# Performance work log

Measured on AMD Instinct MI355X. Metric: run time of the kernel, lower is better.

## Reference

```python
import jax, jax.numpy as jnp
import numpy as np

B, T, D, H = 32, 4096, 512, 512


def setup_inputs() -> dict:
    key = jax.random.key(0)
    ks = jax.random.split(key, 8)
    s = 1.0 / np.sqrt(D)
    return {
        "hidden_state": jax.random.normal(ks[0], (B, D), jnp.float32),
        "encoder_outputs": jax.random.normal(ks[1], (B, T, D), jnp.float32),
        "W": jax.random.normal(ks[2], (D, H), jnp.float32) * s,
        "U": jax.random.normal(ks[3], (D, H), jnp.float32) * s,
        "V": jax.random.normal(ks[4], (H,), jnp.float32) * s,
        "bias": jnp.zeros((H,), jnp.float32),
        "Wa": jax.random.normal(ks[5], (H, H), jnp.float32) * (1.0 / np.sqrt(H)),
        "ba": jnp.zeros((H,), jnp.float32),
    }


def reference(hidden_state, encoder_outputs, W, U, V, bias, Wa, ba):
    # dens1: [B,1,H] ; dens2: [B,T,H]
    dens1 = jnp.einsum('bd,dh->bh', hidden_state, W)[:, None, :]
    dens2 = jnp.einsum('btd,dh->bth', encoder_outputs, U)
    pre = dens1 + dens2 + bias                       # [B,T,H]
    tanh_ = jnp.tanh(jnp.einsum('bth,hk->btk', pre, Wa) + ba)  # extra Dense(tanh)
    cij = jnp.einsum('bth,h->bt', tanh_, V)          # [B,T]
    alphas = jax.nn.softmax(cij, axis=-1)            # [B,T]
    output = jnp.einsum('btd,bt->bd', encoder_outputs, alphas)  # weighted sum
    return output, alphas
```

## Files before the change

### kernel.cpp

```cpp
#include <hip/hip_runtime.h>
#include <hip/hip_bf16.h>


#define BB 32
#define TT 4096
#define DD 512
#define HH 512
#define BK 64

typedef short s16x8 __attribute__((ext_vector_type(8)));
typedef float f32x4 __attribute__((ext_vector_type(4)));

union FU { float f; unsigned u; };

static __device__ __forceinline__ unsigned pack_bf16_trunc(float a, float b) {
    FU ua, ub; ua.f = a; ub.f = b;
    return (ua.u >> 16) | (ub.u & 0xffff0000u);
}

static __device__ __forceinline__ unsigned short f2bf_rne(float x) {
    FU v; v.f = x;
    unsigned u = v.u;
    u = u + 0x7fffu + ((u >> 16) & 1u);
    return (unsigned short)(u >> 16);
}

static __device__ __forceinline__ float tanh_fast(float x) {
    float e = __expf(2.0f * x);
    return 1.0f - 2.0f * __builtin_amdgcn_rcpf(e + 1.0f);
}

static __device__ __forceinline__ void gload_lds16(const void* g, void* l) {
    __builtin_amdgcn_global_load_lds(
        (const __attribute__((address_space(1))) unsigned int*)g,
        (__attribute__((address_space(3))) unsigned int*)l, 16, 0, 0);
}

__global__ void k_dens1(const float* __restrict__ hs, const float* __restrict__ W,
                        const float* __restrict__ bias, float* __restrict__ g) {
    int bi = blockIdx.x;
    int dc = bi & 3, hb = (bi >> 2) & 1, b = bi >> 3;
    int h = hb * 256 + threadIdx.x;
    float s = (dc == 0) ? bias[h] : 0.0f;
    int d0 = dc * 128;
    #pragma unroll 4
    for (int d = 0; d < 128; ++d)
        s = fmaf(hs[b * DD + d0 + d], W[(size_t)(d0 + d) * HH + h], s);
    atomicAdd(&g[b * HH + h], s);
}

__global__ void k_cvec(const float* __restrict__ g, const float* __restrict__ Wa,
                       const float* __restrict__ ba, float* __restrict__ cvec) {
    int bi = blockIdx.x;
    int hc = bi & 3, kb = (bi >> 2) & 1, b = bi >> 3;
    int k = kb * 256 + threadIdx.x;
    float s = (hc == 0) ? ba[k] : 0.0f;
    int h0 = hc * 128;
    #pragma unroll 4
    for (int h = 0; h < 128; ++h)
        s = fmaf(g[b * HH + h0 + h], Wa[(size_t)(h0 + h) * HH + k], s);
    atomicAdd(&cvec[b * HH + k], s);
}

__global__ void k_uwa(const float* __restrict__ U, const float* __restrict__ Wa,
                      unsigned short* __restrict__ UWaT) {
    int d0 = blockIdx.x * 8;
    int tid = threadIdx.x;
    __shared__ float Us[8][DD];
    #pragma unroll
    for (int i = 0; i < 16; ++i) {
        int idx = i * 256 + tid;
        Us[idx >> 9][idx & 511] = U[(size_t)(d0 + (idx >> 9)) * HH + (idx & 511)];
    }
    __syncthreads();
    float acc[8][2] = {};
    #pragma unroll 2
    for (int h = 0; h < DD; ++h) {
        float w0 = Wa[(size_t)h * HH + tid];
        float w1 = Wa[(size_t)h * HH + 256 + tid];
        #pragma unroll
        for (int dd = 0; dd < 8; ++dd) {
            float u = Us[dd][h];
            acc[dd][0] = fmaf(u, w0, acc[dd][0]);
            acc[dd][1] = fmaf(u, w1, acc[dd][1]);
        }
    }
    #pragma unroll
    for (int dd = 0; dd < 8; ++dd) {
        UWaT[(size_t)tid * DD + d0 + dd] = f2bf_rne(acc[dd][0]);
        UWaT[(size_t)(tid + 256) * DD + d0 + dd] = f2bf_rne(acc[dd][1]);
    }
}

__global__ void __launch_bounds__(512, 2) k_gemm_tanh(
    const float* __restrict__ e, const unsigned short* __restrict__ Bt,
    const float* __restrict__ cvec, const float* __restrict__ V,
    float* __restrict__ cij) {
    int tid = threadIdx.x;
    int m0 = blockIdx.x * 128;
    int lane = tid & 63, w = tid >> 6;
    int wr = w >> 2, wc = w & 3;
    int wm = wr * 64, wn = wc * 128;
    int lcol = lane & 15, q = lane >> 4;
    int rl = lane >> 3, gg = lane & 7;

    __shared__ __align__(16) unsigned short As[128 * BK];
    __shared__ __align__(16) unsigned short Bs[512 * BK];

    f32x4 acc[4][8] = {};

    const float* Abase = e + (size_t)m0 * DD;

    for (int k0 = 0; k0 < DD; k0 += BK) {
        float4 av[4];
        #pragma unroll
        for (int it = 0; it < 4; ++it) {
            int idx = it * 512 + tid;
            int row = idx >> 4, c4 = idx & 15;
            av[it] = *(const float4*)(Abase + (size_t)row * DD + k0 + c4 * 4);
        }
        #pragma unroll
        for (int u = 0; u < 8; ++u) {
            int n0 = w * 64 + u * 8;
            const unsigned short* gp =
                Bt + (size_t)(n0 + rl) * DD + k0 + ((gg ^ rl) << 3);
            gload_lds16(gp, &Bs[n0 * 64]);
        }
        #pragma unroll
        for (int it = 0; it < 4; ++it) {
            int idx = it * 512 + tid;
            int row = idx >> 4, c4 = idx & 15;
            uint2 wv;
            wv.x = pack_bf16_trunc(av[it].x, av[it].y);
            wv.y = pack_bf16_trunc(av[it].z, av[it].w);
            int g = c4 >> 1, half = c4 & 1;
            *(uint2*)&As[(g * 128 + (row ^ g)) * 8 + half * 4] = wv;
        }
        __syncthreads();
        #pragma unroll
        for (int ks = 0; ks < BK; ks += 32) {
            int gk = ks >> 3;
            s16x8 af[4], bfr[8];
            #pragma unroll
            for (int i = 0; i < 4; ++i) {
                int row = wm + i * 16 + lcol, g = gk + q;
                af[i] = *(const s16x8*)&As[(g * 128 + (row ^ g)) * 8];
            }
            #pragma unroll
            for (int j = 0; j < 8; ++j) {
                int col = wn + j * 16 + lcol, g = gk + q;
                bfr[j] = *(const s16x8*)&Bs[col * 64 + ((g ^ (col & 7)) << 3)];
            }
            #pragma unroll
            for (int i = 0; i < 4; ++i)
                #pragma unroll
                for (int j = 0; j < 8; ++j)
                    acc[i][j] = __builtin_amdgcn_mfma_f32_16x16x32_bf16(
                        af[i], bfr[j], acc[i][j], 0, 0, 0);
        }
        __syncthreads();
    }

    int b = m0 >> 12;
    float cvv[8], Vv[8];
    #pragma unroll
    for (int j = 0; j < 8; ++j) {
        int h = wn + j * 16 + lcol;
        cvv[j] = cvec[b * HH + h];
        Vv[j] = V[h];
    }
    #pragma unroll
    for (int i = 0; i < 4; ++i) {
        #pragma unroll
        for (int r = 0; r < 4; ++r) {
            float s = 0.0f;
            #pragma unroll
            for (int j = 0; j < 8; ++j)
                s = fmaf(tanh_fast(acc[i][j][r] + cvv[j]), Vv[j], s);
            s += __shfl_xor(s, 1);
            s += __shfl_xor(s, 2);
            s += __shfl_xor(s, 4);
            s += __shfl_xor(s, 8);
            if (lcol == 0)
                atomicAdd(&cij[m0 + wm + i * 16 + q * 4 + r], s);
        }
    }
}

__global__ void k_softmax(const float* __restrict__ cij, float* __restrict__ alphas) {
    int b = blockIdx.x, tid = threadIdx.x;
    const float* row = cij + (size_t)b * TT;
    __shared__ float red[4];
    float m = -1e30f;
    for (int t = tid; t < TT; t += 256) m = fmaxf(m, row[t]);
    #pragma unroll
    for (int o = 1; o < 64; o <<= 1) m = fmaxf(m, __shfl_xor(m, o));
    if ((tid & 63) == 0) red[tid >> 6] = m;
    __syncthreads();
    m = fmaxf(fmaxf(red[0], red[1]), fmaxf(red[2], red[3]));
    __syncthreads();
    float sum = 0.0f;
    for (int t = tid; t < TT; t += 256) sum += __expf(row[t] - m);
    #pragma unroll
    for (int o = 1; o < 64; o <<= 1) sum += __shfl_xor(sum, o);
    if ((tid & 63) == 0) red[tid >> 6] = sum;
    __syncthreads();
    float inv = 1.0f / (red[0] + red[1] + red[2] + red[3]);
    for (int t = tid; t < TT; t += 256)
        alphas[(size_t)b * TT + t] = __expf(row[t] - m) * inv;
}

__global__ void k_wsum(const float* __restrict__ e, const float* __restrict__ alphas,
                       float* __restrict__ pw) {
    int b = blockIdx.x >> 6;
    int chunk = blockIdx.x & 63;
    int t0 = chunk * 64;
    int tid = threadIdx.x;
    int half = tid >> 7, f4 = tid & 127;
    const float* base = e + (size_t)b * TT * DD;
    const float* al = alphas + (size_t)b * TT;
    f32x4 a0 = {0, 0, 0, 0}, a1 = {0, 0, 0, 0};
    for (int it = 0; it < 16; ++it) {
        int t = t0 + it * 4 + half;
        float w0 = al[t], w1 = al[t + 2];
        f32x4 v0 = *(const f32x4*)(base + (size_t)t * DD + f4 * 4);
        f32x4 v1 = *(const f32x4*)(base + (size_t)(t + 2) * DD + f4 * 4);
        a0 += w0 * v0;
        a1 += w1 * v1;
    }
    a0 += a1;
    __shared__ f32x4 red[128];
    if (half == 1) red[f4] = a0;
    __syncthreads();
    if (half == 0) {
        a0 += red[f4];
        *(f32x4*)&pw[((size_t)(b * 64 + chunk)) * DD + f4 * 4] = a0;
    }
}

__global__ void k_wred(const float* __restrict__ pw, float* __restrict__ out) {
    int b = blockIdx.x, tid = threadIdx.x;
    float2 acc = {0.0f, 0.0f};
    const float* base = pw + (size_t)b * 64 * DD;
    #pragma unroll 4
    for (int c = 0; c < 64; ++c) {
        float2 v = *(const float2*)(base + (size_t)c * DD + tid * 2);
        acc.x += v.x;
        acc.y += v.y;
    }
    *(float2*)&out[b * DD + tid * 2] = acc;
}

extern "C" void kernel_launch(void* const* d_in, const int* in_sizes, int n_in,
                              void* d_out, int out_size, void* d_ws, size_t ws_size,
                              hipStream_t stream) {
    const float* hs   = (const float*)d_in[0];
    const float* e    = (const float*)d_in[1];
    const float* W    = (const float*)d_in[2];
    const float* U    = (const float*)d_in[3];
    const float* V    = (const float*)d_in[4];
    const float* bias = (const float*)d_in[5];
    const float* Wa   = (const float*)d_in[6];
    const float* ba   = (const float*)d_in[7];

    float* out    = (float*)d_out;
    float* alphas = out + BB * DD;

    float*          cij  = (float*)d_ws;
    float*          g    = (float*)((char*)d_ws + 524288);
    float*          cvec = (float*)((char*)d_ws + 589824);
    unsigned short* Bt   = (unsigned short*)((char*)d_ws + 655360);
    float*          pw   = (float*)((char*)d_ws + 1179648);

    hipMemsetAsync(d_ws, 0, 655360, stream);

    k_dens1<<<256, 256, 0, stream>>>(hs, W, bias, g);
    k_cvec<<<256, 256, 0, stream>>>(g, Wa, ba, cvec);
    k_uwa<<<64, 256, 0, stream>>>(U, Wa, Bt);
    k_gemm_tanh<<<1024, 512, 0, stream>>>(e, Bt, cvec, V, cij);
    k_softmax<<<BB, 256, 0, stream>>>(cij, alphas);
    k_wsum<<<BB * 64, 256, 0, stream>>>(e, alphas, pw);
    k_wred<<<BB, 256, 0, stream>>>(pw, out);
}
```

Measured before the change: 569.3 us.

## Fuse local softmax and weighted sum into GEMM epilogue, merge prologue kernels

The GEMM-tanh kernel now reduces scores within the block through LDS instead of atomics. It computes a per-tile max and exp-sum and forms a partial weighted sum of the encoder rows it just processed, so the separate full pass over encoder_outputs is gone. A final kernel rescales the per-tile partials with the global max to produce the output and alphas. The dens1/cvec/UWa precompute kernels are merged into one launch, and the workspace memset is removed. The cost is a longer GEMM epilogue that re-reads the tile's fp32 rows, which may or may not hit in cache.

Result: faster. 516.0 us (-9.4%).

```diff
diff --git a/kernel.cpp b/kernel.cpp
--- a/kernel.cpp
+++ b/kernel.cpp
@@ -36,66 +36,72 @@
         (__attribute__((address_space(3))) unsigned int*)l, 16, 0, 0);
 }
 
-__global__ void k_dens1(const float* __restrict__ hs, const float* __restrict__ W,
-                        const float* __restrict__ bias, float* __restrict__ g) {
-    int bi = blockIdx.x;
-    int dc = bi & 3, hb = (bi >> 2) & 1, b = bi >> 3;
-    int h = hb * 256 + threadIdx.x;
-    float s = (dc == 0) ? bias[h] : 0.0f;
-    int d0 = dc * 128;
-    #pragma unroll 4
-    for (int d = 0; d < 128; ++d)
-        s = fmaf(hs[b * DD + d0 + d], W[(size_t)(d0 + d) * HH + h], s);
-    atomicAdd(&g[b * HH + h], s);
-}
-
-__global__ void k_cvec(const float* __restrict__ g, const float* __restrict__ Wa,
-                       const float* __restrict__ ba, float* __restrict__ cvec) {
-    int bi = blockIdx.x;
-    int hc = bi & 3, kb = (bi >> 2) & 1, b = bi >> 3;
-    int k = kb * 256 + threadIdx.x;
-    float s = (hc == 0) ? ba[k] : 0.0f;
-    int h0 = hc * 128;
-    #pragma unroll 4
-    for (int h = 0; h < 128; ++h)
-        s = fmaf(g[b * HH + h0 + h], Wa[(size_t)(h0 + h) * HH + k], s);
-    atomicAdd(&cvec[b * HH + k], s);
-}
-
-__global__ void k_uwa(const float* __restrict__ U, const float* __restrict__ Wa,
-                      unsigned short* __restrict__ UWaT) {
-    int d0 = blockIdx.x * 8;
+__global__ void k_pre(const float* __restrict__ U, const float* __restrict__ Wa,
+                      unsigned short* __restrict__ UWaT,
+                      const float* __restrict__ hs, const float* __restrict__ W,
+                      const float* __restrict__ bias, const float* __restrict__ ba,
+                      float* __restrict__ cvec) {
+    __shared__ float smem[8 * DD];
     int tid = threadIdx.x;
-    __shared__ float Us[8][DD];
-    #pragma unroll
-    for (int i = 0; i < 16; ++i) {
-        int idx = i * 256 + tid;
-        Us[idx >> 9][idx & 511] = U[(size_t)(d0 + (idx >> 9)) * HH + (idx & 511)];
-    }
-    __syncthreads();
-    float acc[8][2] = {};
-    #pragma unroll 2
-    for (int h = 0; h < DD; ++h) {
-        float w0 = Wa[(size_t)h * HH + tid];
-        float w1 = Wa[(size_t)h * HH + 256 + tid];
+    if (blockIdx.x < 64) {
+        int d0 = blockIdx.x * 8;
+        float (*Us)[DD] = (float(*)[DD])smem;
+        #pragma unroll
+        for (int i = 0; i < 16; ++i) {
+            int idx = i * 256 + tid;
+            Us[idx >> 9][idx & 511] = U[(size_t)(d0 + (idx >> 9)) * HH + (idx & 511)];
+        }
+        __syncthreads();
+        float acc[8][2] = {};
+        #pragma unroll 2
+        for (int h = 0; h < DD; ++h) {
+            float w0 = Wa[(size_t)h * HH + tid];
+            float w1 = Wa[(size_t)h * HH + 256 + tid];
+            #pragma unroll
+            for (int dd = 0; dd < 8; ++dd) {
+                float u = Us[dd][h];
+                acc[dd][0] = fmaf(u, w0, acc[dd][0]);
+                acc[dd][1] = fmaf(u, w1, acc[dd][1]);
+            }
+        }
         #pragma unroll
         for (int dd = 0; dd < 8; ++dd) {
-            float u = Us[dd][h];
-            acc[dd][0] = fmaf(u, w0, acc[dd][0]);
-            acc[dd][1] = fmaf(u, w1, acc[dd][1]);
-        }
-    }
-    #pragma unroll
-    for (int dd = 0; dd < 8; ++dd) {
-        UWaT[(size_t)tid * DD + d0 + dd] = f2bf_rne(acc[dd][0]);
-        UWaT[(size_t)(tid + 256) * DD + d0 + dd] = f2bf_rne(acc[dd][1]);
+            UWaT[(size_t)tid * DD + d0 + dd] = f2bf_rne(acc[dd][0]);
+            UWaT[(size_t)(tid + 256) * DD + d0 + dd] = f2bf_rne(acc[dd][1]);
+        }
+    } else {
+        int b = blockIdx.x - 64;
+        float* hss = smem;
+        float* gs = smem + DD;
+        if (tid < 128)
+            ((float4*)hss)[tid] = ((const float4*)(hs + (size_t)b * DD))[tid];
+        __syncthreads();
+        float a0 = bias[tid], a1 = bias[tid + 256];
+        #pragma unroll 8
+        for (int d = 0; d < DD; ++d) {
+            float x = hss[d];
+            a0 = fmaf(x, W[(size_t)d * HH + tid], a0);
+            a1 = fmaf(x, W[(size_t)d * HH + 256 + tid], a1);
+        }
+        gs[tid] = a0;
+        gs[tid + 256] = a1;
+        __syncthreads();
+        float c0 = ba[tid], c1 = ba[tid + 256];
+        #pragma unroll 8
+        for (int h = 0; h < HH; ++h) {
+            float x = gs[h];
+            c0 = fmaf(x, Wa[(size_t)h * HH + tid], c0);
+            c1 = fmaf(x, Wa[(size_t)h * HH + 256 + tid], c1);
+        }
+        cvec[(size_t)b * HH + tid] = c0;
+        cvec[(size_t)b * HH + 256 + tid] = c1;
     }
 }
 
 __global__ void __launch_bounds__(512, 2) k_gemm_tanh(
     const float* __restrict__ e, const unsigned short* __restrict__ Bt,
     const float* __restrict__ cvec, const float* __restrict__ V,
-    float* __restrict__ cij) {
+    float* __restrict__ cij, float* __restrict__ pw, float* __restrict__ mz) {
     int tid = threadIdx.x;
     int m0 = blockIdx.x * 128;
     int lane = tid & 63, w = tid >> 6;
@@ -106,9 +112,9 @@
 
     __shared__ __align__(16) unsigned short As[128 * BK];
     __shared__ __align__(16) unsigned short Bs[512 * BK];
+    __shared__ float red2[4];
 
     f32x4 acc[4][8] = {};
-
     const float* Abase = e + (size_t)m0 * DD;
 
     for (int k0 = 0; k0 < DD; k0 += BK) {
@@ -122,9 +128,8 @@
         #pragma unroll
         for (int u = 0; u < 8; ++u) {
             int n0 = w * 64 + u * 8;
-            const unsigned short* gp =
-                Bt + (size_t)(n0 + rl) * DD + k0 + ((gg ^ rl) << 3);
-            gload_lds16(gp, &Bs[n0 * 64]);
+            gload_lds16(Bt + (size_t)(n0 + rl) * DD + k0 + ((gg ^ rl) << 3),
+                        &Bs[n0 * 64]);
         }
         #pragma unroll
         for (int it = 0; it < 4; ++it) {
@@ -169,6 +174,8 @@
         cvv[j] = cvec[b * HH + h];
         Vv[j] = V[h];
     }
+    float* redf = (float*)As;
+    float* wbuf = (float*)Bs;
     #pragma unroll
     for (int i = 0; i < 4; ++i) {
         #pragma unroll
@@ -182,73 +189,82 @@
             s += __shfl_xor(s, 4);
             s += __shfl_xor(s, 8);
             if (lcol == 0)
-                atomicAdd(&cij[m0 + wm + i * 16 + q * 4 + r], s);
-        }
-    }
-}
-
-__global__ void k_softmax(const float* __restrict__ cij, float* __restrict__ alphas) {
+                redf[(wm + i * 16 + q * 4 + r) * 4 + wc] = s;
+        }
+    }
+    __syncthreads();
+
+    float v = 0.0f;
+    if (tid < 128) {
+        v = redf[tid * 4] + redf[tid * 4 + 1] + redf[tid * 4 + 2] + redf[tid * 4 + 3];
+        cij[m0 + tid] = v;
+        float mm = v;
+        #pragma unroll
+        for (int o = 1; o < 64; o <<= 1) mm = fmaxf(mm, __shfl_xor(mm, o));
+        if (lane == 0) red2[tid >> 6] = mm;
+    }
+    __syncthreads();
+    float m_c = fmaxf(red2[0], red2[1]);
+    if (tid < 128) {
+        float wv = __expf(v - m_c);
+        wbuf[tid] = wv;
+        float ss = wv;
+        #pragma unroll
+        for (int o = 1; o < 64; o <<= 1) ss += __shfl_xor(ss, o);
+        if (lane == 0) red2[2 + (tid >> 6)] = ss;
+    }
+    __syncthreads();
+    if (tid == 0) {
+        mz[blockIdx.x * 2] = m_c;
+        mz[blockIdx.x * 2 + 1] = red2[2] + red2[3];
+    }
+
+    float pacc = 0.0f;
+    const float* ecol = e + (size_t)m0 * DD + tid;
+    #pragma unroll 8
+    for (int t = 0; t < 128; ++t)
+        pacc = fmaf(wbuf[t], ecol[(size_t)t * DD], pacc);
+    pw[(size_t)blockIdx.x * DD + tid] = pacc;
+}
+
+__global__ void k_final(const float* __restrict__ cij, const float* __restrict__ pw,
+                        const float* __restrict__ mz, float* __restrict__ alphas,
+                        float* __restrict__ out) {
     int b = blockIdx.x, tid = threadIdx.x;
-    const float* row = cij + (size_t)b * TT;
-    __shared__ float red[4];
-    float m = -1e30f;
-    for (int t = tid; t < TT; t += 256) m = fmaxf(m, row[t]);
+    __shared__ float ef[32];
+    __shared__ float red[2];
+    float m = (tid < 32) ? mz[(size_t)(b * 32 + tid) * 2] : -1e30f;
+    if (tid < 64) {
+        #pragma unroll
+        for (int o = 1; o < 64; o <<= 1) m = fmaxf(m, __shfl_xor(m, o));
+        if (tid == 0) red[0] = m;
+    }
+    __syncthreads();
+    float M = red[0];
+    if (tid < 64) {
+        float z = 0.0f;
+        if (tid < 32) {
+            float e_ = __expf(mz[(size_t)(b * 32 + tid) * 2] - M);
+            ef[tid] = e_;
+            z = e_ * mz[(size_t)(b * 32 + tid) * 2 + 1];
+        }
+        #pragma unroll
+        for (int o = 1; o < 64; o <<= 1) z += __shfl_xor(z, o);
+        if (tid == 0) red[1] = z;
+    }
+    __syncthreads();
+    float inv = 1.0f / red[1];
     #pragma unroll
-    for (int o = 1; o < 64; o <<= 1) m = fmaxf(m, __shfl_xor(m, o));
-    if ((tid & 63) == 0) red[tid >> 6] = m;
-    __syncthreads();
-    m = fmaxf(fmaxf(red[0], red[1]), fmaxf(red[2], red[3]));
-    __syncthreads();
-    float sum = 0.0f;
-    for (int t = tid; t < TT; t += 256) sum += __expf(row[t] - m);
-    #pragma unroll
-    for (int o = 1; o < 64; o <<= 1) sum += __shfl_xor(sum, o);
-    if ((tid & 63) == 0) red[tid >> 6] = sum;
-    __syncthreads();
-    float inv = 1.0f / (red[0] + red[1] + red[2] + red[3]);
+    for (int d = tid; d < DD; d += 256) {
+        float s = 0.0f;
+        #pragma unroll 8
+        for (int c = 0; c < 32; ++c)
+            s = fmaf(ef[c], pw[(size_t)(b * 32 + c) * DD + d], s);
+        out[(size_t)b * DD + d] = s * inv;
+    }
+    const float* crow = cij + (size_t)b * TT;
     for (int t = tid; t < TT; t += 256)
-        alphas[(size_t)b * TT + t] = __expf(row[t] - m) * inv;
-}
-
-__global__ void k_wsum(const float* __restrict__ e, const float* __restrict__ alphas,
-                       float* __restrict__ pw) {
-    int b = blockIdx.x >> 6;
-    int chunk = blockIdx.x & 63;
-    int t0 = chunk * 64;
-    int tid = threadIdx.x;
-    int half = tid >> 7, f4 = tid & 127;
-    const float* base = e + (size_t)b * TT * DD;
-    const float* al = alphas + (size_t)b * TT;
-    f32x4 a0 = {0, 0, 0, 0}, a1 = {0, 0, 0, 0};
-    for (int it = 0; it < 16; ++it) {
-        int t = t0 + it * 4 + half;
-        float w0 = al[t], w1 = al[t + 2];
-        f32x4 v0 = *(const f32x4*)(base + (size_t)t * DD + f4 * 4);
-        f32x4 v1 = *(const f32x4*)(base + (size_t)(t + 2) * DD + f4 * 4);
-        a0 += w0 * v0;
-        a1 += w1 * v1;
-    }
-    a0 += a1;
-    __shared__ f32x4 red[128];
-    if (half == 1) red[f4] = a0;
-    __syncthreads();
-    if (half == 0) {
-        a0 += red[f4];
-        *(f32x4*)&pw[((size_t)(b * 64 + chunk)) * DD + f4 * 4] = a0;
-    }
-}
-
-__global__ void k_wred(const float* __restrict__ pw, float* __restrict__ out) {
-    int b = blockIdx.x, tid = threadIdx.x;
-    float2 acc = {0.0f, 0.0f};
-    const float* base = pw + (size_t)b * 64 * DD;
-    #pragma unroll 4
-    for (int c = 0; c < 64; ++c) {
-        float2 v = *(const float2*)(base + (size_t)c * DD + tid * 2);
-        acc.x += v.x;
-        acc.y += v.y;
-    }
-    *(float2*)&out[b * DD + tid * 2] = acc;
+        alphas[(size_t)b * TT + t] = __expf(crow[t] - M) * inv;
 }
 
 extern "C" void kernel_launch(void* const* d_in, const int* in_sizes, int n_in,
@@ -267,18 +283,12 @@
     float* alphas = out + BB * DD;
 
     float*          cij  = (float*)d_ws;
-    float*          g    = (float*)((char*)d_ws + 524288);
-    float*          cvec = (float*)((char*)d_ws + 589824);
-    unsigned short* Bt   = (unsigned short*)((char*)d_ws + 655360);
-    float*          pw   = (float*)((char*)d_ws + 1179648);
-
-    hipMemsetAsync(d_ws, 0, 655360, stream);
-
-    k_dens1<<<256, 256, 0, stream>>>(hs, W, bias, g);
-    k_cvec<<<256, 256, 0, stream>>>(g, Wa, ba, cvec);
-    k_uwa<<<64, 256, 0, stream>>>(U, Wa, Bt);
-    k_gemm_tanh<<<1024, 512, 0, stream>>>(e, Bt, cvec, V, cij);
-    k_softmax<<<BB, 256, 0, stream>>>(cij, alphas);
-    k_wsum<<<BB * 64, 256, 0, stream>>>(e, alphas, pw);
-    k_wred<<<BB, 256, 0, stream>>>(pw, out);
-}
+    float*          cvec = (float*)((char*)d_ws + 524288);
+    unsigned short* Bt   = (unsigned short*)((char*)d_ws + 589824);
+    float*          mz   = (float*)((char*)d_ws + 1114112);
+    float*          pw   = (float*)((char*)d_ws + 1122304);
+
+    k_pre<<<96, 256, 0, stream>>>(U, Wa, Bt, hs, W, bias, ba, cvec);
+    k_gemm_tanh<<<1024, 512, 0, stream>>>(e, Bt, cvec, V, cij, pw, mz);
+    k_final<<<BB, 256, 0, stream>>>(cij, pw, mz, alphas, out);
+}
```
